# Performance work log

Measured on AMD Instinct MI355X. Metric: run time of the kernel, lower is better.

Reference implementation:

```python
import jax, jax.numpy as jnp
import numpy as np

NUM_FREQUENCIES = 128
NUM_TIMES = 128
SIGMA = 0.1
BATCH = 32
LENGTH = 8192


def setup_inputs() -> dict:
    key = jax.random.key(0)
    signal = jax.random.normal(key, (BATCH, LENGTH), dtype=jnp.float32)
    return {"signal": signal}


def reference(signal) -> jnp.ndarray:
    # signal: [B, L]
    B, L = signal.shape
    # Matches torch.linspace(...).long(): linspace then truncate toward zero.
    time_centers = jnp.linspace(0.0, L - 1, NUM_TIMES).astype(jnp.int32).astype(jnp.float32)  # [T]
    freq_vals = jnp.linspace(0.0, L // 2, NUM_FREQUENCIES).astype(jnp.int32).astype(jnp.float32)  # [F]
    t = jnp.arange(L, dtype=jnp.float32)  # [L]
    sigma_w = SIGMA * L
    # Gaussian windows, one per time center: [T, L]
    window = jnp.exp(-0.5 * ((t[None, :] - time_centers[:, None]) / sigma_w) ** 2)
    # Real part of exp(-2j*pi*f*l/L) modulation: [F, L]
    two_pi = jnp.float32(2.0 * np.pi)
    cos_mod = jnp.cos(two_pi * freq_vals[:, None] * t[None, :] / L)
    # Original loop stores a complex dot product into a real tensor -> real part only:
    # result[b, f, t] = sum_l signal[b,l] * window[t,l] * cos(2*pi*f*l/L)
    windowed = jnp.einsum('bl,tl->btl', signal, window)  # [B, T, L]
    result = jnp.einsum('btl,fl->bft', windowed, cos_mod)  # [B, F, T]
    return result
```

## Files before the change

### kernel.cpp

```cpp
#include <hip/hip_runtime.h>
#include <hip/hip_bf16.h>
#include <math.h>


#define L_ 8192
#define B_ 32

typedef _Float16 half8 __attribute__((ext_vector_type(8)));
typedef __fp16 fp16x2 __attribute__((ext_vector_type(2)));
typedef float float2v __attribute__((ext_vector_type(2)));
typedef float float4v __attribute__((ext_vector_type(4)));

#define H_ 0.001220703125f
#define CSTEP_ 7.66990393942594528198e-4f

__global__ __launch_bounds__(512, 4) void gabor_kernel(
    const float* __restrict__ signal, float* __restrict__ out) {
  const int bx = blockIdx.x;
  const int b = bx & 31;
  const int th = (bx >> 5) & 3;
  const int fh = (bx >> 7) & 3;
  const int tid = threadIdx.x;
  const int lane = tid & 63;
  const int wv = tid >> 6;
  const int frow = lane & 15;
  const int quad = lane >> 4;

  __shared__ __align__(16) char smraw[32768];
  _Float16* Sg = (_Float16*)smraw;
  float4v (*Acc)[64][4] = (float4v(*)[64][4])smraw;

  {
    const float* srow = signal + (size_t)b * L_;
#pragma unroll
    for (int i = 0; i < 2; ++i) {
      const int off = i * 4096 + tid * 8;
      float4v s0 = *(const float4v*)(srow + off);
      float4v s1 = *(const float4v*)(srow + off + 4);
      union { fp16x2 h2[4]; half8 h8; } sh;
      sh.h2[0] = __builtin_amdgcn_cvt_pkrtz(s0[0], s0[1]);
      sh.h2[1] = __builtin_amdgcn_cvt_pkrtz(s0[2], s0[3]);
      sh.h2[2] = __builtin_amdgcn_cvt_pkrtz(s1[0], s1[1]);
      sh.h2[3] = __builtin_amdgcn_cvt_pkrtz(s1[2], s1[3]);
      *(half8*)&Sg[off] = sh.h8;
    }
  }
  __syncthreads();

  const int t0 = th * 32;
  const int f0 = fh * 32;
  const int k0 = wv * 1024 + quad * 8;

  float2v w2[2][4], Rw2[2][4];
  float2v cE2[2][4], cO2[2][4];
  float2v K32v[2];
  const float2v Q32v = {0.99847528338432312012f,
                        0.99847528338432312012f};
#pragma unroll
  for (int fr = 0; fr < 2; ++fr) {
    const float tc = truncf((float)(t0 + fr * 16 + frow) * (8191.0f / 127.0f));
    const int fv = (int)((float)(f0 + fr * 16 + frow) * (4096.0f / 127.0f));
    const float K32 = 2.0f * __cosf((float)((fv * 32) & (L_ - 1)) * CSTEP_);
    K32v[fr] = (float2v){K32, K32};
#pragma unroll
    for (int q = 0; q < 4; ++q) {
#pragma unroll
      for (int h = 0; h < 2; ++h) {
        const int j = 2 * q + h;
        const float x = ((float)(k0 + j) - tc) * H_;
        w2[fr][q][h] = __expf(-0.5f * x * x);
        Rw2[fr][q][h] =
            __expf(__builtin_fmaf(-0.0390625f, x, -7.62939453125e-4f));
        cE2[fr][q][h] = __cosf((float)((fv * (k0 + j)) & (L_ - 1)) * CSTEP_);
        cO2[fr][q][h] =
            __cosf((float)((fv * (k0 + j + 8160)) & (L_ - 1)) * CSTEP_);
      }
    }
  }

  float4v acc[2][2];
#pragma unroll
  for (int i = 0; i < 2; ++i)
#pragma unroll
    for (int j = 0; j < 2; ++j) acc[i][j] = (float4v)(0.0f);

  union H8 { fp16x2 h2[4]; half8 h8; };

#pragma unroll 1
  for (int p = 0; p < 16; ++p) {
    {
      H8 ha[2], hc[2];
#pragma unroll
      for (int fr = 0; fr < 2; ++fr)
#pragma unroll
        for (int q = 0; q < 4; ++q) {
          ha[fr].h2[q] = __builtin_amdgcn_cvt_pkrtz(w2[fr][q][0], w2[fr][q][1]);
          hc[fr].h2[q] = __builtin_amdgcn_cvt_pkrtz(cE2[fr][q][0], cE2[fr][q][1]);
        }
      const half8 sgv = *(const half8*)&Sg[k0 + (2 * p) * 32];
#pragma unroll
      for (int fr2 = 0; fr2 < 2; ++fr2) {
        const half8 hbf = hc[fr2].h8 * sgv;
        acc[0][fr2] = __builtin_amdgcn_mfma_f32_16x16x32_f16(ha[0].h8, hbf,
                                                             acc[0][fr2], 0, 0, 0);
        acc[1][fr2] = __builtin_amdgcn_mfma_f32_16x16x32_f16(ha[1].h8, hbf,
                                                             acc[1][fr2], 0, 0, 0);
      }
#pragma unroll
      for (int fr = 0; fr < 2; ++fr)
#pragma unroll
        for (int q = 0; q < 4; ++q) {
          w2[fr][q] *= Rw2[fr][q];
          Rw2[fr][q] *= Q32v;
          cO2[fr][q] = __builtin_elementwise_fma(K32v[fr], cE2[fr][q], -cO2[fr][q]);
        }
    }
    {
      H8 ha[2], hc[2];
#pragma unroll
      for (int fr = 0; fr < 2; ++fr)
#pragma unroll
        for (int q = 0; q < 4; ++q) {
          ha[fr].h2[q] = __builtin_amdgcn_cvt_pkrtz(w2[fr][q][0], w2[fr][q][1]);
          hc[fr].h2[q] = __builtin_amdgcn_cvt_pkrtz(cO2[fr][q][0], cO2[fr][q][1]);
        }
      const half8 sgv = *(const half8*)&Sg[k0 + (2 * p + 1) * 32];
#pragma unroll
      for (int fr2 = 0; fr2 < 2; ++fr2) {
        const half8 hbf = hc[fr2].h8 * sgv;
        acc[0][fr2] = __builtin_amdgcn_mfma_f32_16x16x32_f16(ha[0].h8, hbf,
                                                             acc[0][fr2], 0, 0, 0);
        acc[1][fr2] = __builtin_amdgcn_mfma_f32_16x16x32_f16(ha[1].h8, hbf,
                                                             acc[1][fr2], 0, 0, 0);
      }
#pragma unroll
      for (int fr = 0; fr < 2; ++fr)
#pragma unroll
        for (int q = 0; q < 4; ++q) {
          w2[fr][q] *= Rw2[fr][q];
          Rw2[fr][q] *= Q32v;
          cE2[fr][q] = __builtin_elementwise_fma(K32v[fr], cO2[fr][q], -cE2[fr][q]);
        }
    }
  }

  __syncthreads();
#pragma unroll
  for (int i4 = 0; i4 < 4; ++i4)
    Acc[wv][lane][i4] = acc[i4 >> 1][i4 & 1];
  __syncthreads();
  if (wv < 4) {
    float4v sum = Acc[0][lane][wv];
#pragma unroll
    for (int w = 1; w < 8; ++w) sum += Acc[w][lane][wv];
    const int fr1 = wv >> 1, fr2 = wv & 1;
    const int f = f0 + fr2 * 16 + frow;
    const int t = t0 + fr1 * 16 + quad * 4;
    *(float4v*)(out + ((size_t)(b * 128 + f)) * 128 + t) = sum;
  }
}

extern "C" void kernel_launch(void* const* d_in, const int* in_sizes, int n_in,
                              void* d_out, int out_size, void* d_ws, size_t ws_size,
                              hipStream_t stream) {
  const float* signal = (const float*)d_in[0];
  float* out = (float*)d_out;
  gabor_kernel<<<dim3(512), dim3(512), 0, stream>>>(signal, out);
}
```

Baseline: 72.11 us.

## Process two batch rows per block to reuse window/cosine operands

Each block now handles two batch signals, staging both in shared memory and reusing the generated Gaussian window and cosine fragments across them, which doubles the MFMA work per recurrence update. The grid halves to 256 blocks and the launch-bounds occupancy hint drops to 2 blocks per CU to allow more accumulator registers. The aim is to amortise the per-step VALU recurrence and conversion cost. The trade-off is fewer blocks, which is below the CU count on MI355X and leaves some CUs idle, plus higher register pressure.

Result: faster. 68.03 us (-5.7%).

```diff
diff --git a/kernel.cpp b/kernel.cpp
--- a/kernel.cpp
+++ b/kernel.cpp
@@ -14,12 +14,12 @@
 #define H_ 0.001220703125f
 #define CSTEP_ 7.66990393942594528198e-4f
 
-__global__ __launch_bounds__(512, 4) void gabor_kernel(
+__global__ __launch_bounds__(512, 2) void gabor_kernel(
     const float* __restrict__ signal, float* __restrict__ out) {
   const int bx = blockIdx.x;
-  const int b = bx & 31;
-  const int th = (bx >> 5) & 3;
-  const int fh = (bx >> 7) & 3;
+  const int bp = bx & 15;
+  const int th = (bx >> 4) & 3;
+  const int fh = (bx >> 6) & 3;
   const int tid = threadIdx.x;
   const int lane = tid & 63;
   const int wv = tid >> 6;
@@ -27,22 +27,25 @@
   const int quad = lane >> 4;
 
   __shared__ __align__(16) char smraw[32768];
-  _Float16* Sg = (_Float16*)smraw;
-  float4v (*Acc)[64][4] = (float4v(*)[64][4])smraw;
+  _Float16(*Sg)[L_] = (_Float16(*)[L_])smraw;
+  float4v(*Acc)[64][4] = (float4v(*)[64][4])smraw;
 
   {
-    const float* srow = signal + (size_t)b * L_;
 #pragma unroll
-    for (int i = 0; i < 2; ++i) {
-      const int off = i * 4096 + tid * 8;
-      float4v s0 = *(const float4v*)(srow + off);
-      float4v s1 = *(const float4v*)(srow + off + 4);
-      union { fp16x2 h2[4]; half8 h8; } sh;
-      sh.h2[0] = __builtin_amdgcn_cvt_pkrtz(s0[0], s0[1]);
-      sh.h2[1] = __builtin_amdgcn_cvt_pkrtz(s0[2], s0[3]);
-      sh.h2[2] = __builtin_amdgcn_cvt_pkrtz(s1[0], s1[1]);
-      sh.h2[3] = __builtin_amdgcn_cvt_pkrtz(s1[2], s1[3]);
-      *(half8*)&Sg[off] = sh.h8;
+    for (int bi = 0; bi < 2; ++bi) {
+      const float* srow = signal + (size_t)(2 * bp + bi) * L_;
+#pragma unroll
+      for (int i = 0; i < 2; ++i) {
+        const int off = i * 4096 + tid * 8;
+        float4v s0 = *(const float4v*)(srow + off);
+        float4v s1 = *(const float4v*)(srow + off + 4);
+        union { fp16x2 h2[4]; half8 h8; } sh;
+        sh.h2[0] = __builtin_amdgcn_cvt_pkrtz(s0[0], s0[1]);
+        sh.h2[1] = __builtin_amdgcn_cvt_pkrtz(s0[2], s0[3]);
+        sh.h2[2] = __builtin_amdgcn_cvt_pkrtz(s1[0], s1[1]);
+        sh.h2[3] = __builtin_amdgcn_cvt_pkrtz(s1[2], s1[3]);
+        *(half8*)&Sg[bi][off] = sh.h8;
+      }
     }
   }
   __syncthreads();
@@ -78,11 +81,13 @@
     }
   }
 
-  float4v acc[2][2];
+  float4v acc[2][2][2];
 #pragma unroll
   for (int i = 0; i < 2; ++i)
 #pragma unroll
-    for (int j = 0; j < 2; ++j) acc[i][j] = (float4v)(0.0f);
+    for (int j = 0; j < 2; ++j)
+#pragma unroll
+      for (int bi = 0; bi < 2; ++bi) acc[i][j][bi] = (float4v)(0.0f);
 
   union H8 { fp16x2 h2[4]; half8 h8; };
 
@@ -97,14 +102,21 @@
           ha[fr].h2[q] = __builtin_amdgcn_cvt_pkrtz(w2[fr][q][0], w2[fr][q][1]);
           hc[fr].h2[q] = __builtin_amdgcn_cvt_pkrtz(cE2[fr][q][0], cE2[fr][q][1]);
         }
-      const half8 sgv = *(const half8*)&Sg[k0 + (2 * p) * 32];
+      const int kk = k0 + (2 * p) * 32;
+      const half8 sg0 = *(const half8*)&Sg[0][kk];
+      const half8 sg1 = *(const half8*)&Sg[1][kk];
 #pragma unroll
       for (int fr2 = 0; fr2 < 2; ++fr2) {
-        const half8 hbf = hc[fr2].h8 * sgv;
-        acc[0][fr2] = __builtin_amdgcn_mfma_f32_16x16x32_f16(ha[0].h8, hbf,
-                                                             acc[0][fr2], 0, 0, 0);
-        acc[1][fr2] = __builtin_amdgcn_mfma_f32_16x16x32_f16(ha[1].h8, hbf,
-                                                             acc[1][fr2], 0, 0, 0);
+        const half8 hb0 = hc[fr2].h8 * sg0;
+        const half8 hb1 = hc[fr2].h8 * sg1;
+        acc[0][fr2][0] = __builtin_amdgcn_mfma_f32_16x16x32_f16(
+            ha[0].h8, hb0, acc[0][fr2][0], 0, 0, 0);
+        acc[1][fr2][0] = __builtin_amdgcn_mfma_f32_16x16x32_f16(
+            ha[1].h8, hb0, acc[1][fr2][0], 0, 0, 0);
+        acc[0][fr2][1] = __builtin_amdgcn_mfma_f32_16x16x32_f16(
+            ha[0].h8, hb1, acc[0][fr2][1], 0, 0, 0);
+        acc[1][fr2][1] = __builtin_amdgcn_mfma_f32_16x16x32_f16(
+            ha[1].h8, hb1, acc[1][fr2][1], 0, 0, 0);
       }
 #pragma unroll
       for (int fr = 0; fr < 2; ++fr)
@@ -124,14 +136,21 @@
           ha[fr].h2[q] = __builtin_amdgcn_cvt_pkrtz(w2[fr][q][0], w2[fr][q][1]);
           hc[fr].h2[q] = __builtin_amdgcn_cvt_pkrtz(cO2[fr][q][0], cO2[fr][q][1]);
         }
-      const half8 sgv = *(const half8*)&Sg[k0 + (2 * p + 1) * 32];
+      const int kk = k0 + (2 * p + 1) * 32;
+      const half8 sg0 = *(const half8*)&Sg[0][kk];
+      const half8 sg1 = *(const half8*)&Sg[1][kk];
 #pragma unroll
       for (int fr2 = 0; fr2 < 2; ++fr2) {
-        const half8 hbf = hc[fr2].h8 * sgv;
-        acc[0][fr2] = __builtin_amdgcn_mfma_f32_16x16x32_f16(ha[0].h8, hbf,
-                                                             acc[0][fr2], 0, 0, 0);
-        acc[1][fr2] = __builtin_amdgcn_mfma_f32_16x16x32_f16(ha[1].h8, hbf,
-                                                             acc[1][fr2], 0, 0, 0);
+        const half8 hb0 = hc[fr2].h8 * sg0;
+        const half8 hb1 = hc[fr2].h8 * sg1;
+        acc[0][fr2][0] = __builtin_amdgcn_mfma_f32_16x16x32_f16(
+            ha[0].h8, hb0, acc[0][fr2][0], 0, 0, 0);
+        acc[1][fr2][0] = __builtin_amdgcn_mfma_f32_16x16x32_f16(
+            ha[1].h8, hb0, acc[1][fr2][0], 0, 0, 0);
+        acc[0][fr2][1] = __builtin_amdgcn_mfma_f32_16x16x32_f16(
+            ha[0].h8, hb1, acc[0][fr2][1], 0, 0, 0);
+        acc[1][fr2][1] = __builtin_amdgcn_mfma_f32_16x16x32_f16(
+            ha[1].h8, hb1, acc[1][fr2][1], 0, 0, 0);
       }
 #pragma unroll
       for (int fr = 0; fr < 2; ++fr)
@@ -144,19 +163,22 @@
     }
   }
 
-  __syncthreads();
 #pragma unroll
-  for (int i4 = 0; i4 < 4; ++i4)
-    Acc[wv][lane][i4] = acc[i4 >> 1][i4 & 1];
-  __syncthreads();
-  if (wv < 4) {
-    float4v sum = Acc[0][lane][wv];
+  for (int bi = 0; bi < 2; ++bi) {
+    __syncthreads();
 #pragma unroll
-    for (int w = 1; w < 8; ++w) sum += Acc[w][lane][wv];
-    const int fr1 = wv >> 1, fr2 = wv & 1;
-    const int f = f0 + fr2 * 16 + frow;
-    const int t = t0 + fr1 * 16 + quad * 4;
-    *(float4v*)(out + ((size_t)(b * 128 + f)) * 128 + t) = sum;
+    for (int i4 = 0; i4 < 4; ++i4)
+      Acc[wv][lane][i4] = acc[i4 >> 1][i4 & 1][bi];
+    __syncthreads();
+    if (wv < 4) {
+      float4v sum = Acc[0][lane][wv];
+#pragma unroll
+      for (int w = 1; w < 8; ++w) sum += Acc[w][lane][wv];
+      const int fr1 = wv >> 1, fr2 = wv & 1;
+      const int f = f0 + fr2 * 16 + frow;
+      const int t = t0 + fr1 * 16 + quad * 4;
+      *(float4v*)(out + ((size_t)((2 * bp + bi) * 128 + f)) * 128 + t) = sum;
+    }
   }
 }
 
@@ -165,5 +187,5 @@
                               hipStream_t stream) {
   const float* signal = (const float*)d_in[0];
   float* out = (float*)d_out;
-  gabor_kernel<<<dim3(512), dim3(512), 0, stream>>>(signal, out);
+  gabor_kernel<<<dim3(256), dim3(512), 0, stream>>>(signal, out);
 }
```

## Share generated window/cosine fragments across four batches and split K across blocks

Applied to the files above, without the earlier changes.

Each block now handles four batch rows and half of the L dimension, so the expensive on-the-fly window and cosine recurrence values are reused across four batches instead of being regenerated per batch. The K dimension is split in two across blocks, with partial results combined through atomicAdd into an output zeroed by a memset. This cuts the VALU generation work per MFMA, but it needs more accumulator registers (occupancy bound lowered to 2), halves the grid to 256 blocks, and adds atomics and a memset launch.

After: 79.59 us. 1.1x slower.

```diff
diff --git a/kernel.cpp b/kernel.cpp
--- a/kernel.cpp
+++ b/kernel.cpp
@@ -14,12 +14,13 @@
 #define H_ 0.001220703125f
 #define CSTEP_ 7.66990393942594528198e-4f
 
-__global__ __launch_bounds__(512, 4) void gabor_kernel(
+__global__ __launch_bounds__(512, 2) void gabor_kernel(
     const float* __restrict__ signal, float* __restrict__ out) {
   const int bx = blockIdx.x;
-  const int b = bx & 31;
-  const int th = (bx >> 5) & 3;
-  const int fh = (bx >> 7) & 3;
+  const int kh = bx & 1;
+  const int fh = (bx >> 1) & 3;
+  const int th = (bx >> 3) & 3;
+  const int bq = (bx >> 5) & 7;
   const int tid = threadIdx.x;
   const int lane = tid & 63;
   const int wv = tid >> 6;
@@ -27,29 +28,28 @@
   const int quad = lane >> 4;
 
   __shared__ __align__(16) char smraw[32768];
-  _Float16* Sg = (_Float16*)smraw;
-  float4v (*Acc)[64][4] = (float4v(*)[64][4])smraw;
+  _Float16(*Sg)[4096] = (_Float16(*)[4096])smraw;
+  float4v(*Acc)[64][4] = (float4v(*)[64][4])smraw;
 
-  {
-    const float* srow = signal + (size_t)b * L_;
 #pragma unroll
-    for (int i = 0; i < 2; ++i) {
-      const int off = i * 4096 + tid * 8;
-      float4v s0 = *(const float4v*)(srow + off);
-      float4v s1 = *(const float4v*)(srow + off + 4);
-      union { fp16x2 h2[4]; half8 h8; } sh;
-      sh.h2[0] = __builtin_amdgcn_cvt_pkrtz(s0[0], s0[1]);
-      sh.h2[1] = __builtin_amdgcn_cvt_pkrtz(s0[2], s0[3]);
-      sh.h2[2] = __builtin_amdgcn_cvt_pkrtz(s1[0], s1[1]);
-      sh.h2[3] = __builtin_amdgcn_cvt_pkrtz(s1[2], s1[3]);
-      *(half8*)&Sg[off] = sh.h8;
-    }
+  for (int bi = 0; bi < 4; ++bi) {
+    const float* srow =
+        signal + (size_t)(4 * bq + bi) * L_ + kh * 4096 + tid * 8;
+    float4v s0 = *(const float4v*)srow;
+    float4v s1 = *(const float4v*)(srow + 4);
+    union { fp16x2 h2[4]; half8 h8; } sh;
+    sh.h2[0] = __builtin_amdgcn_cvt_pkrtz(s0[0], s0[1]);
+    sh.h2[1] = __builtin_amdgcn_cvt_pkrtz(s0[2], s0[3]);
+    sh.h2[2] = __builtin_amdgcn_cvt_pkrtz(s1[0], s1[1]);
+    sh.h2[3] = __builtin_amdgcn_cvt_pkrtz(s1[2], s1[3]);
+    *(half8*)&Sg[bi][tid * 8] = sh.h8;
   }
   __syncthreads();
 
   const int t0 = th * 32;
   const int f0 = fh * 32;
-  const int k0 = wv * 1024 + quad * 8;
+  const int kloc0 = wv * 512 + quad * 8;
+  const int k0g = kh * 4096 + kloc0;
 
   float2v w2[2][4], Rw2[2][4];
   float2v cE2[2][4], cO2[2][4];
@@ -67,27 +67,36 @@
 #pragma unroll
       for (int h = 0; h < 2; ++h) {
         const int j = 2 * q + h;
-        const float x = ((float)(k0 + j) - tc) * H_;
+        const float x = ((float)(k0g + j) - tc) * H_;
         w2[fr][q][h] = __expf(-0.5f * x * x);
         Rw2[fr][q][h] =
             __expf(__builtin_fmaf(-0.0390625f, x, -7.62939453125e-4f));
-        cE2[fr][q][h] = __cosf((float)((fv * (k0 + j)) & (L_ - 1)) * CSTEP_);
+        cE2[fr][q][h] = __cosf((float)((fv * (k0g + j)) & (L_ - 1)) * CSTEP_);
         cO2[fr][q][h] =
-            __cosf((float)((fv * (k0 + j + 8160)) & (L_ - 1)) * CSTEP_);
+            __cosf((float)((fv * (k0g + j + 8160)) & (L_ - 1)) * CSTEP_);
       }
     }
   }
 
-  float4v acc[2][2];
+  float4v acc[4][2][2];
 #pragma unroll
-  for (int i = 0; i < 2; ++i)
+  for (int bi = 0; bi < 4; ++bi)
 #pragma unroll
-    for (int j = 0; j < 2; ++j) acc[i][j] = (float4v)(0.0f);
+    for (int i = 0; i < 2; ++i)
+#pragma unroll
+      for (int j = 0; j < 2; ++j) acc[bi][i][j] = (float4v)(0.0f);
 
   union H8 { fp16x2 h2[4]; half8 h8; };
 
 #pragma unroll 1
-  for (int p = 0; p < 16; ++p) {
+  for (int p = 0; p < 8; ++p) {
+    half8 sgE[4], sgO[4];
+    const int kkE = kloc0 + (2 * p) * 32;
+#pragma unroll
+    for (int bi = 0; bi < 4; ++bi) {
+      sgE[bi] = *(const half8*)&Sg[bi][kkE];
+      sgO[bi] = *(const half8*)&Sg[bi][kkE + 32];
+    }
     {
       H8 ha[2], hc[2];
 #pragma unroll
@@ -97,15 +106,6 @@
           ha[fr].h2[q] = __builtin_amdgcn_cvt_pkrtz(w2[fr][q][0], w2[fr][q][1]);
           hc[fr].h2[q] = __builtin_amdgcn_cvt_pkrtz(cE2[fr][q][0], cE2[fr][q][1]);
         }
-      const half8 sgv = *(const half8*)&Sg[k0 + (2 * p) * 32];
-#pragma unroll
-      for (int fr2 = 0; fr2 < 2; ++fr2) {
-        const half8 hbf = hc[fr2].h8 * sgv;
-        acc[0][fr2] = __builtin_amdgcn_mfma_f32_16x16x32_f16(ha[0].h8, hbf,
-                                                             acc[0][fr2], 0, 0, 0);
-        acc[1][fr2] = __builtin_amdgcn_mfma_f32_16x16x32_f16(ha[1].h8, hbf,
-                                                             acc[1][fr2], 0, 0, 0);
-      }
 #pragma unroll
       for (int fr = 0; fr < 2; ++fr)
 #pragma unroll
@@ -114,6 +114,17 @@
           Rw2[fr][q] *= Q32v;
           cO2[fr][q] = __builtin_elementwise_fma(K32v[fr], cE2[fr][q], -cO2[fr][q]);
         }
+#pragma unroll
+      for (int bi = 0; bi < 4; ++bi) {
+#pragma unroll
+        for (int fr2 = 0; fr2 < 2; ++fr2) {
+          const half8 hbf = hc[fr2].h8 * sgE[bi];
+          acc[bi][0][fr2] = __builtin_amdgcn_mfma_f32_16x16x32_f16(
+              ha[0].h8, hbf, acc[bi][0][fr2], 0, 0, 0);
+          acc[bi][1][fr2] = __builtin_amdgcn_mfma_f32_16x16x32_f16(
+              ha[1].h8, hbf, acc[bi][1][fr2], 0, 0, 0);
+        }
+      }
     }
     {
       H8 ha[2], hc[2];
@@ -124,15 +135,6 @@
           ha[fr].h2[q] = __builtin_amdgcn_cvt_pkrtz(w2[fr][q][0], w2[fr][q][1]);
           hc[fr].h2[q] = __builtin_amdgcn_cvt_pkrtz(cO2[fr][q][0], cO2[fr][q][1]);
         }
-      const half8 sgv = *(const half8*)&Sg[k0 + (2 * p + 1) * 32];
-#pragma unroll
-      for (int fr2 = 0; fr2 < 2; ++fr2) {
-        const half8 hbf = hc[fr2].h8 * sgv;
-        acc[0][fr2] = __builtin_amdgcn_mfma_f32_16x16x32_f16(ha[0].h8, hbf,
-                                                             acc[0][fr2], 0, 0, 0);
-        acc[1][fr2] = __builtin_amdgcn_mfma_f32_16x16x32_f16(ha[1].h8, hbf,
-                                                             acc[1][fr2], 0, 0, 0);
-      }
 #pragma unroll
       for (int fr = 0; fr < 2; ++fr)
 #pragma unroll
@@ -141,22 +143,38 @@
           Rw2[fr][q] *= Q32v;
           cE2[fr][q] = __builtin_elementwise_fma(K32v[fr], cO2[fr][q], -cE2[fr][q]);
         }
+#pragma unroll
+      for (int bi = 0; bi < 4; ++bi) {
+#pragma unroll
+        for (int fr2 = 0; fr2 < 2; ++fr2) {
+          const half8 hbf = hc[fr2].h8 * sgO[bi];
+          acc[bi][0][fr2] = __builtin_amdgcn_mfma_f32_16x16x32_f16(
+              ha[0].h8, hbf, acc[bi][0][fr2], 0, 0, 0);
+          acc[bi][1][fr2] = __builtin_amdgcn_mfma_f32_16x16x32_f16(
+              ha[1].h8, hbf, acc[bi][1][fr2], 0, 0, 0);
+        }
+      }
     }
   }
 
-  __syncthreads();
 #pragma unroll
-  for (int i4 = 0; i4 < 4; ++i4)
-    Acc[wv][lane][i4] = acc[i4 >> 1][i4 & 1];
-  __syncthreads();
-  if (wv < 4) {
-    float4v sum = Acc[0][lane][wv];
+  for (int bi = 0; bi < 4; ++bi) {
+    __syncthreads();
 #pragma unroll
-    for (int w = 1; w < 8; ++w) sum += Acc[w][lane][wv];
-    const int fr1 = wv >> 1, fr2 = wv & 1;
-    const int f = f0 + fr2 * 16 + frow;
-    const int t = t0 + fr1 * 16 + quad * 4;
-    *(float4v*)(out + ((size_t)(b * 128 + f)) * 128 + t) = sum;
+    for (int i4 = 0; i4 < 4; ++i4)
+      Acc[wv][lane][i4] = acc[bi][i4 >> 1][i4 & 1];
+    __syncthreads();
+    if (wv < 4) {
+      float4v sum = Acc[0][lane][wv];
+#pragma unroll
+      for (int w = 1; w < 8; ++w) sum += Acc[w][lane][wv];
+      const int fr1 = wv >> 1, fr2 = wv & 1;
+      const int f = f0 + fr2 * 16 + frow;
+      const int t = t0 + fr1 * 16 + quad * 4;
+      float* o = out + ((size_t)((4 * bq + bi) * 128 + f)) * 128 + t;
+#pragma unroll
+      for (int r = 0; r < 4; ++r) atomicAdd(o + r, sum[r]);
+    }
   }
 }
 
@@ -165,5 +183,6 @@
                               hipStream_t stream) {
   const float* signal = (const float*)d_in[0];
   float* out = (float*)d_out;
-  gabor_kernel<<<dim3(512), dim3(512), 0, stream>>>(signal, out);
+  hipMemsetAsync(out, 0, (size_t)out_size * sizeof(float), stream);
+  gabor_kernel<<<dim3(256), dim3(512), 0, stream>>>(signal, out);
 }
```
